# Kernel optimization log

Hardware: AMD Instinct MI355X
Metric: run time of the kernel (lower is better)

The kernel has to match this reference:

```python
import jax, jax.numpy as jnp
import numpy as np

T, B, D, H, F, E = 2048, 2, 1024, 16, 4096, 8
HD = D // H


def layer_norm(x, g, b, eps=1e-5):
    m = x.mean(-1, keepdims=True)
    v = ((x - m) ** 2).mean(-1, keepdims=True)
    return (x - m) * jax.lax.rsqrt(v + eps) * g + b


def setup_inputs() -> dict:
    key = jax.random.key(0)
    ks = jax.random.split(key, 24)
    s = 0.02
    inp = {
        "x": jax.random.normal(ks[0], (T, B, D), jnp.float32),
        # self-attention (fairseq MultiheadAttention)
        "Wq": jax.random.normal(ks[1], (D, D), jnp.float32) * s,
        "bq": jnp.zeros((D,), jnp.float32),
        "Wk": jax.random.normal(ks[2], (D, D), jnp.float32) * s,
        "bk": jnp.zeros((D,), jnp.float32),
        "Wv": jax.random.normal(ks[3], (D, D), jnp.float32) * s,
        "bv": jnp.zeros((D,), jnp.float32),
        "Wo": jax.random.normal(ks[4], (D, D), jnp.float32) * s,
        "bo": jnp.zeros((D,), jnp.float32),
        "ln1_g": jnp.ones((D,), jnp.float32),
        "ln1_b": jnp.zeros((D,), jnp.float32),
        "ln2_g": jnp.ones((D,), jnp.float32),
        "ln2_b": jnp.zeros((D,), jnp.float32),
        # MoE: expert_centroids Linear(D -> E, bias=False) => weight [E, D]
        "cent": jax.random.normal(ks[5], (E, D), jnp.float32) * s,
        # per-expert MoESublayer params (base_sublayers=1)
        "e_ln_g": jnp.ones((E, D), jnp.float32),
        "e_ln_b": jnp.zeros((E, D), jnp.float32),
        "e_W1": jax.random.normal(ks[6], (E, D, F), jnp.float32) * s,
        "e_b1": jnp.zeros((E, F), jnp.float32),
        "e_W2": jax.random.normal(ks[7], (E, F, D), jnp.float32) * s,
        "e_b2": jnp.zeros((E, D), jnp.float32),
    }
    return inp


def reference(x, Wq, bq, Wk, bk, Wv, bv, Wo, bo, ln1_g, ln1_b, ln2_g, ln2_b,
              cent, e_ln_g, e_ln_b, e_W1, e_b1, e_W2, e_b2):
    # ---- self-attention block (pre-norm, causal) ----
    res = x  # [T,B,D]
    h = layer_norm(x, ln1_g, ln1_b)
    q = ((h @ Wq) + bq) * (HD ** -0.5)
    k = h @ Wk + bk
    v = h @ Wv + bv
    q = q.reshape(T, B, H, HD)
    k = k.reshape(T, B, H, HD)
    v = v.reshape(T, B, H, HD)
    scores = jnp.einsum('tbhd,sbhd->bhts', q, k)
    causal = jnp.tril(jnp.ones((T, T), bool))
    scores = jnp.where(causal, scores, -1e9)
    p = jax.nn.softmax(scores, axis=-1)
    a = jnp.einsum('bhts,sbhd->tbhd', p, v).reshape(T, B, D)
    x = res + (a @ Wo + bo)

    # ---- MoE block (pre-norm) ----
    res = x
    h = layer_norm(x, ln2_g, ln2_b)
    # MoELayer: transpose(0,1) then flatten -> [B*T, D] token-major by batch
    xs = h.transpose(1, 0, 2).reshape(B * T, D)
    logits = xs.astype(jnp.float32) @ cent.T  # fp32 gating, [N,E]
    assign = jnp.argmax(logits, axis=-1)      # greedy top-1 routing

    # single-device semantics: All2All identity; sort + inverse-sort cancel,
    # so out[t] = expert_{assign[t]}(xs[t]). Compute each expert densely and select.
    def sublayer(g, b, W1, b1, W2, b2):
        hh = jax.nn.relu(layer_norm(xs, g, b) @ W1 + b1)  # [N,F]
        return xs + hh @ W2 + b2                          # internal residual

    ys = jax.vmap(sublayer)(e_ln_g, e_ln_b, e_W1, e_b1, e_W2, e_b2)  # [E,N,D]
    moe_out = jnp.take_along_axis(ys, assign[None, :, None], axis=0)[0]  # [N,D]
    moe_out = moe_out.reshape(B, T, D).transpose(1, 0, 2)  # back to [T,B,D]

    return res + moe_out
```

## Files before the change

kernel.cpp:

```cpp
#include <hip/hip_runtime.h>
#include <hip/hip_bf16.h>
#include <math.h>

#define T_ 2048
#define B_ 2
#define D_ 1024
#define H_ 16
#define F_ 4096
#define E_ 8
#define N_ 4096
#define HD_ 64
#define PADROWS 5120

typedef __attribute__((ext_vector_type(8))) short short8_t;
typedef __attribute__((ext_vector_type(4))) float f32x4_t;
typedef __attribute__((ext_vector_type(16))) float f32x16_t;
typedef __attribute__((ext_vector_type(4))) unsigned u32x4_t;

__device__ __forceinline__ unsigned short f2bf(float f) {
    union { float f; unsigned u; } a; a.f = f;
    unsigned r = a.u + 0x7FFFu + ((a.u >> 16) & 1u);
    return (unsigned short)(r >> 16);
}

__device__ __forceinline__ unsigned cvtpk(float lo, float hi) {
    unsigned r;
    asm("v_cvt_pk_bf16_f32 %0, %1, %2" : "=v"(r) : "v"(lo), "v"(hi));
    return r;
}

__device__ __forceinline__ void glds16(const unsigned short* g, unsigned short* l) {
    __builtin_amdgcn_global_load_lds(
        (const __attribute__((address_space(1))) void*)g,
        (__attribute__((address_space(3))) void*)l, 16, 0, 0);
}

__device__ __forceinline__ void blockReduce2(float& a, float& b, float* sm) {
    #pragma unroll
    for (int m = 32; m; m >>= 1) { a += __shfl_xor(a, m); b += __shfl_xor(b, m); }
    const int w = threadIdx.x >> 6, l = threadIdx.x & 63;
    __syncthreads();
    if (l == 0) { sm[w] = a; sm[8 + w] = b; }
    __syncthreads();
    a = sm[0] + sm[1] + sm[2] + sm[3];
    b = sm[8] + sm[9] + sm[10] + sm[11];
}

__global__ __launch_bounds__(256) void k_transpose(const float* __restrict__ in,
                                                   unsigned short* __restrict__ out,
                                                   int R, int C) {
    __shared__ float tile[32][33];
    const int c0 = blockIdx.x * 32, r0 = blockIdx.y * 32;
    const size_t base = (size_t)blockIdx.z * R * C;
    in += base; out += base;
    const int tx = threadIdx.x & 31, ty = threadIdx.x >> 5;
    #pragma unroll
    for (int i = 0; i < 32; i += 8)
        tile[ty + i][tx] = in[(size_t)(r0 + ty + i) * C + c0 + tx];
    __syncthreads();
    const int c = threadIdx.x >> 3, rq = (threadIdx.x & 7) * 4;
    ushort4 v;
    v.x = f2bf(tile[rq + 0][c]);
    v.y = f2bf(tile[rq + 1][c]);
    v.z = f2bf(tile[rq + 2][c]);
    v.w = f2bf(tile[rq + 3][c]);
    *(ushort4*)(out + (size_t)(c0 + c) * R + r0 + rq) = v;
}

__global__ __launch_bounds__(256) void k_transpose_v(const unsigned short* __restrict__ in,
                                                     unsigned short* __restrict__ out) {
    const int bh = blockIdx.x;
    const int t0 = blockIdx.y * 128;
    const int tid = threadIdx.x;
    const int hd = tid & 63;
    const size_t ib = (size_t)bh * T_ * HD_;
    const size_t ob = (size_t)bh * HD_ * T_;
    for (int tb = tid >> 6; tb < 16; tb += 4) {
        const int t = t0 + tb * 8;
        short8_t v;
        #pragma unroll
        for (int k = 0; k < 8; ++k)
            v[k] = (short)in[ib + (size_t)(t + k) * HD_ + hd];
        *(short8_t*)(out + ob + (size_t)hd * T_ + t) = v;
    }
}

__global__ __launch_bounds__(256) void k_ln(const float* __restrict__ x,
                                            const float* __restrict__ g,
                                            const float* __restrict__ b,
                                            unsigned short* __restrict__ out) {
    __shared__ float sm[16];
    const int row = blockIdx.x, tid = threadIdx.x;
    const float4 v = *(const float4*)(x + (size_t)row * D_ + tid * 4);
    float s1 = v.x + v.y + v.z + v.w;
    float s2 = v.x * v.x + v.y * v.y + v.z * v.z + v.w * v.w;
    blockReduce2(s1, s2, sm);
    const float mean = s1 * (1.f / D_);
    const float inv  = rsqrtf(s2 * (1.f / D_) - mean * mean + 1e-5f);
    const float4 gg = *(const float4*)(g + tid * 4);
    const float4 bb = *(const float4*)(b + tid * 4);
    unsigned long long pk =
          (unsigned long long)f2bf((v.x - mean) * inv * gg.x + bb.x)
        | ((unsigned long long)f2bf((v.y - mean) * inv * gg.y + bb.y) << 16)
        | ((unsigned long long)f2bf((v.z - mean) * inv * gg.z + bb.z) << 32)
        | ((unsigned long long)f2bf((v.w - mean) * inv * gg.w + bb.w) << 48);
    *(unsigned long long*)(out + (size_t)row * D_ + tid * 4) = pk;
}

__global__ __launch_bounds__(256) void k_init_x2(const float* __restrict__ x,
                                                 const float* __restrict__ bo,
                                                 float* __restrict__ x2) {
    const int row = blockIdx.x, tid = threadIdx.x;
    const size_t idx = (size_t)row * D_ + tid * 4;
    const float4 v = *(const float4*)(x + idx);
    const float4 b = *(const float4*)(bo + tid * 4);
    float4 o; o.x = v.x + b.x; o.y = v.y + b.y; o.z = v.z + b.z; o.w = v.w + b.w;
    *(float4*)(x2 + idx) = o;
}

__global__ __launch_bounds__(256) void k_init_out(const float* __restrict__ x2u,
                                                  const float* __restrict__ eb2,
                                                  const int* __restrict__ assign,
                                                  float* __restrict__ out) {
    const int row = blockIdx.x, tid = threadIdx.x;
    const int e = assign[row];
    const size_t idx = (size_t)row * D_ + tid * 4;
    const float4 v = *(const float4*)(x2u + idx);
    const float4 b = *(const float4*)(eb2 + (size_t)e * D_ + tid * 4);
    float4 o; o.x = v.x + b.x; o.y = v.y + b.y; o.z = v.z + b.z; o.w = v.w + b.w;
    *(float4*)(out + idx) = o;
}

__device__ __forceinline__ void gemm_core(const unsigned short* ap0, const unsigned short* ap1,
                                          const unsigned short* bp0, const unsigned short* bp1,
                                          int K, unsigned short* Als, unsigned short* Bls,
                                          f32x4_t (&acc)[4][4]) {
    const int tid = threadIdx.x, w = tid >> 6, l = tid & 63;
    const int wm = (w >> 1) * 64, wn = (w & 1) * 64;
    const int fr = l & 15, fg = (l >> 4) * 8;
    const int fgs = fg ^ (((fr >> 1) & 3) << 3);
    f32x4_t z4 = {0.f, 0.f, 0.f, 0.f};
    #pragma unroll
    for (int m = 0; m < 4; m++)
        #pragma unroll
        for (int n = 0; n < 4; n++) acc[m][n] = z4;
    glds16(ap0, Als + w * 512);
    glds16(ap1, Als + (w + 4) * 512);
    glds16(bp0, Bls + w * 512);
    glds16(bp1, Bls + (w + 4) * 512);
    ap0 += 32; ap1 += 32; bp0 += 32; bp1 += 32;
    glds16(ap0, Als + 4096 + w * 512);
    glds16(ap1, Als + 4096 + (w + 4) * 512);
    glds16(bp0, Bls + 4096 + w * 512);
    glds16(bp1, Bls + 4096 + (w + 4) * 512);
    ap0 += 32; ap1 += 32; bp0 += 32; bp1 += 32;
    unsigned c0 = 0, c1 = 4096, c2 = 8192;
    const int nk = K >> 5;
    for (int kt = 0; kt < nk; ++kt) {
        if (kt < nk - 1) asm volatile("s_waitcnt vmcnt(4)" ::: "memory");
        else             asm volatile("s_waitcnt vmcnt(0)" ::: "memory");
        __builtin_amdgcn_s_barrier();
        __builtin_amdgcn_sched_barrier(0);
        short8_t a[4], b[4];
        #pragma unroll
        for (int m = 0; m < 4; m++) a[m] = *(const short8_t*)(Als + c0 + (wm + m * 16 + fr) * 32 + fgs);
        #pragma unroll
        for (int n = 0; n < 4; n++) b[n] = *(const short8_t*)(Bls + c0 + (wn + n * 16 + fr) * 32 + fgs);
        #pragma unroll
        for (int m = 0; m < 4; m++)
            #pragma unroll
            for (int n = 0; n < 4; n++)
                acc[m][n] = __builtin_amdgcn_mfma_f32_16x16x32_bf16(a[m], b[n], acc[m][n], 0, 0, 0);
        if (kt + 2 < nk) {
            glds16(ap0, Als + c2 + w * 512);
            glds16(ap1, Als + c2 + (w + 4) * 512);
            glds16(bp0, Bls + c2 + w * 512);
            glds16(bp1, Bls + c2 + (w + 4) * 512);
            ap0 += 32; ap1 += 32; bp0 += 32; bp1 += 32;
        }
        const unsigned t = c0; c0 = c1; c1 = c2; c2 = t;
    }
}

__global__ __launch_bounds__(256) void k_gemm_qkv(
    const unsigned short* __restrict__ A, const unsigned short* __restrict__ BT,
    const float* __restrict__ bq, const float* __restrict__ bk, const float* __restrict__ bv,
    unsigned short* __restrict__ Qb, unsigned short* __restrict__ Kb, unsigned short* __restrict__ Vb) {
    __shared__ unsigned short Als[12288], Bls[12288];
    const int tid = threadIdx.x, w = tid >> 6, l = tid & 63;
    const int col0 = blockIdx.x * 128, row0 = blockIdx.y * 128;
    const int r0s = w * 16 + (l >> 2), r1s = 64 + w * 16 + (l >> 2);
    const int cs = ((l & 3) ^ ((l >> 3) & 3)) * 8;
    const unsigned short* ap0 = A + (size_t)(row0 + r0s) * D_ + cs;
    const unsigned short* ap1 = A + (size_t)(row0 + r1s) * D_ + cs;
    const unsigned short* bp0 = BT + (size_t)(col0 + r0s) * D_ + cs;
    const unsigned short* bp1 = BT + (size_t)(col0 + r1s) * D_ + cs;
    f32x4_t acc[4][4];
    gemm_core(ap0, ap1, bp0, bp1, D_, Als, Bls, acc);
    const int wm = (w >> 1) * 64, wn = (w & 1) * 64, fr = l & 15, fg4 = l >> 4;
    #pragma unroll
    for (int n = 0; n < 4; n++) {
        const int gcol = col0 + wn + n * 16 + fr;
        const int which = gcol >> 10, dc = gcol & 1023;
        const float bias = which == 0 ? bq[dc] : (which == 1 ? bk[dc] : bv[dc]);
        unsigned short* dst = which == 0 ? Qb : (which == 1 ? Kb : Vb);
        const int hh = dc >> 6, hd = dc & 63;
        #pragma unroll
        for (int m = 0; m < 4; m++)
            #pragma unroll
            for (int rr = 0; rr < 4; rr++) {
                const int grow = row0 + wm + m * 16 + fg4 * 4 + rr;
                float v = acc[m][n][rr] + bias;
                if (which == 0) v *= 0.1803368801111204f;
                const int t = grow >> 1, bb = grow & 1;
                dst[((size_t)(bb * H_ + hh) * T_ + t) * HD_ + hd] = f2bf(v);
            }
    }
}

__global__ __launch_bounds__(256) void k_attn(const unsigned short* __restrict__ Qb,
                                              const unsigned short* __restrict__ Kb,
                                              const unsigned short* __restrict__ Vt,
                                              unsigned short* __restrict__ aout) {
    __shared__ unsigned short Kl[3 * 4096];
    __shared__ unsigned short Vl[3 * 4096];
    const int id = blockIdx.x;
    const int qt = (id < 256) ? (15 - (id & 15)) : (id & 15);
    const int bh = (id >> 4) & 31;
    const int tid = threadIdx.x, w = tid >> 6, l = tid & 63;
    const int q5 = l & 31, hi = l >> 5, l7 = l & 7;
    const int row0 = w * 8 + (l >> 3);
    const int swz = ((l & 7) ^ (l >> 3)) * 8;
    const size_t base = (size_t)bh * T_ * HD_;
    const unsigned short* Qp = Qb + base;
    const unsigned short* kps = Kb + base + (size_t)row0 * HD_ + swz;
    const unsigned short* vps = Vt + base + (size_t)row0 * T_ + swz;
    const int qw0 = qt * 128 + w * 32;
    const int q = qw0 + q5;

    short8_t aq[4];
    #pragma unroll
    for (int khd = 0; khd < 4; ++khd)
        aq[khd] = *(const short8_t*)(Qp + (size_t)q * HD_ + khd * 16 + hi * 8);

    f32x16_t accO0, accO1;
    #pragma unroll
    for (int i = 0; i < 16; ++i) { accO0[i] = 0.f; accO1[i] = 0.f; }
    float mrun = -1e30f, lrun = 0.f;

    const int niter = (qt + 1) * 2;

#define STAGE_KV(t, b) { \
    const size_t ko = (size_t)(t) * 64 * HD_; const int vo = (t) * 64; \
    glds16(kps + ko,            Kl + (b) + w * 512); \
    glds16(kps + ko + 32 * HD_, Kl + (b) + 2048 + w * 512); \
    glds16(vps + vo,            Vl + (b) + w * 512); \
    glds16(vps + vo + 32 * T_,  Vl + (b) + 2048 + w * 512); }

    STAGE_KV(0, 0);
    STAGE_KV(1, 4096);
    unsigned c0 = 0, c1 = 4096, c2 = 8192;

    for (int it = 0; it < niter; ++it) {
        if (it < niter - 1) asm volatile("s_waitcnt vmcnt(4)" ::: "memory");
        else                asm volatile("s_waitcnt vmcnt(0)" ::: "memory");
        __builtin_amdgcn_s_barrier();
        __builtin_amdgcn_sched_barrier(0);
        const int s0 = it * 64;
        if (s0 <= qw0 + 31) {
            const unsigned short* KT = Kl + c0;
            const unsigned short* VT = Vl + c0;

            f32x16_t st0, st1;
            #pragma unroll
            for (int i = 0; i < 16; ++i) { st0[i] = 0.f; st1[i] = 0.f; }
            #pragma unroll
            for (int khd = 0; khd < 4; ++khd) {
                const int cb = (khd * 16 + hi * 8) ^ (l7 * 8);
                const short8_t k0 = *(const short8_t*)(KT + q5 * 64 + cb);
                const short8_t k1 = *(const short8_t*)(KT + (32 + q5) * 64 + cb);
                st0 = __builtin_amdgcn_mfma_f32_32x32x16_bf16(k0, aq[khd], st0, 0, 0, 0);
                st1 = __builtin_amdgcn_mfma_f32_32x32x16_bf16(k1, aq[khd], st1, 0, 0, 0);
            }

            const bool domask = (s0 + 63 > qw0);
            float pmax = -3e38f;
            #pragma unroll
            for (int r = 0; r < 16; ++r) {
                float v0 = st0[r], v1 = st1[r];
                if (domask) {
                    const int kv0 = s0 + (r & 3) + 8 * (r >> 2) + 4 * hi;
                    if (kv0 > q)      v0 = -1e30f;
                    if (kv0 + 32 > q) v1 = -1e30f;
                }
                st0[r] = v0; st1[r] = v1;
                pmax = fmaxf(pmax, fmaxf(v0, v1));
            }
            pmax = fmaxf(pmax, __shfl_xor(pmax, 32));
            const float mnew = fmaxf(mrun, pmax);
            const float scl = exp2f(mrun - mnew);
            float pt0[16], pt1[16];
            float rs = 0.f;
            #pragma unroll
            for (int r = 0; r < 16; ++r) {
                pt0[r] = exp2f(st0[r] - mnew);
                pt1[r] = exp2f(st1[r] - mnew);
                rs += pt0[r] + pt1[r];
            }
            rs += __shfl_xor(rs, 32);
            lrun = lrun * scl + rs;
            mrun = mnew;
            #pragma unroll
            for (int i = 0; i < 16; ++i) { accO0[i] *= scl; accO1[i] *= scl; }

            unsigned Wp[2][4][2];
            #pragma unroll
            for (int b = 0; b < 4; ++b) {
                Wp[0][b][0] = cvtpk(pt0[4 * b + 0], pt0[4 * b + 1]);
                Wp[0][b][1] = cvtpk(pt0[4 * b + 2], pt0[4 * b + 3]);
                Wp[1][b][0] = cvtpk(pt1[4 * b + 0], pt1[4 * b + 1]);
                Wp[1][b][1] = cvtpk(pt1[4 * b + 2], pt1[4 * b + 3]);
            }

            #pragma unroll
            for (int ks = 0; ks < 4; ++ks) {
                const int t = ks >> 1, b0 = (ks & 1) * 2;
                const unsigned ownA0 = Wp[t][b0][0],     ownA1 = Wp[t][b0][1];
                const unsigned ownB0 = Wp[t][b0 + 1][0], ownB1 = Wp[t][b0 + 1][1];
                const unsigned send0 = hi ? ownA0 : ownB0;
                const unsigned send1 = hi ? ownA1 : ownB1;
                const unsigned recv0 = __shfl_xor(send0, 32);
                const unsigned recv1 = __shfl_xor(send1, 32);
                u32x4_t wds;
                wds[0] = hi ? recv0 : ownA0;
                wds[1] = hi ? recv1 : ownA1;
                wds[2] = hi ? ownB0 : recv0;
                wds[3] = hi ? ownB1 : recv1;
                const short8_t pfrag = __builtin_bit_cast(short8_t, wds);
                const int cb = (ks * 16 + hi * 8) ^ (l7 * 8);
                const short8_t v0 = *(const short8_t*)(VT + q5 * 64 + cb);
                const short8_t v1 = *(const short8_t*)(VT + (32 + q5) * 64 + cb);
                accO0 = __builtin_amdgcn_mfma_f32_32x32x16_bf16(v0, pfrag, accO0, 0, 0, 0);
                accO1 = __builtin_amdgcn_mfma_f32_32x32x16_bf16(v1, pfrag, accO1, 0, 0, 0);
            }
        }
        if (it + 2 < niter) STAGE_KV(it + 2, c2);
        const unsigned tb = c0; c0 = c1; c1 = c2; c2 = tb;
    }
#undef STAGE_KV

    const float linv = 1.f / lrun;
    const int bidx = bh >> 4, hidx = bh & 15;
    unsigned short* orow = aout + (size_t)(q * B_ + bidx) * D_ + hidx * 64;
    #pragma unroll
    for (int g = 0; g < 4; ++g) {
        const int hd0 = 8 * g + 4 * hi;
        unsigned long long pk0 =
              (unsigned long long)f2bf(accO0[4 * g + 0] * linv)
            | ((unsigned long long)f2bf(accO0[4 * g + 1] * linv) << 16)
            | ((unsigned long long)f2bf(accO0[4 * g + 2] * linv) << 32)
            | ((unsigned long long)f2bf(accO0[4 * g + 3] * linv) << 48);
        *(unsigned long long*)(orow + hd0) = pk0;
        unsigned long long pk1 =
              (unsigned long long)f2bf(accO1[4 * g + 0] * linv)
            | ((unsigned long long)f2bf(accO1[4 * g + 1] * linv) << 16)
            | ((unsigned long long)f2bf(accO1[4 * g + 2] * linv) << 32)
            | ((unsigned long long)f2bf(accO1[4 * g + 3] * linv) << 48);
        *(unsigned long long*)(orow + 32 + hd0) = pk1;
    }
}

__global__ __launch_bounds__(256) void k_gemm_o(
    const unsigned short* __restrict__ A, const unsigned short* __restrict__ BT,
    float* __restrict__ x2) {
    __shared__ unsigned short Als[12288], Bls[12288];
    const int tid = threadIdx.x, w = tid >> 6, l = tid & 63;
    const int row0 = blockIdx.x * 128, col0 = blockIdx.y * 128;
    const int kc = blockIdx.z * 512;
    const int r0s = w * 16 + (l >> 2), r1s = 64 + w * 16 + (l >> 2);
    const int cs = ((l & 3) ^ ((l >> 3) & 3)) * 8;
    const unsigned short* ap0 = A + (size_t)(row0 + r0s) * D_ + kc + cs;
    const unsigned short* ap1 = A + (size_t)(row0 + r1s) * D_ + kc + cs;
    const unsigned short* bp0 = BT + (size_t)(col0 + r0s) * D_ + kc + cs;
    const unsigned short* bp1 = BT + (size_t)(col0 + r1s) * D_ + kc + cs;
    f32x4_t acc[4][4];
    gemm_core(ap0, ap1, bp0, bp1, 512, Als, Bls, acc);
    const int wm = (w >> 1) * 64, wn = (w & 1) * 64, fr = l & 15, fg4 = l >> 4;
    #pragma unroll
    for (int n = 0; n < 4; n++) {
        const int gcol = col0 + wn + n * 16 + fr;
        #pragma unroll
        for (int m = 0; m < 4; m++)
            #pragma unroll
            for (int rr = 0; rr < 4; rr++) {
                const int grow = row0 + wm + m * 16 + fg4 * 4 + rr;
                atomicAdd(&x2[(size_t)grow * D_ + gcol], acc[m][n][rr]);
            }
    }
}

__global__ __launch_bounds__(256) void k_ln2_gate(
    float* __restrict__ x2, const float* __restrict__ g2, const float* __restrict__ b2,
    const float* __restrict__ cent, const float* __restrict__ eg, const float* __restrict__ eb,
    unsigned short* __restrict__ z, int* __restrict__ assign, int* __restrict__ counts) {
    __shared__ float sm[48];
    const int row = blockIdx.x, tid = threadIdx.x;
    const int w = tid >> 6, l = tid & 63;
    float* xr = x2 + (size_t)row * D_;
    const float4 v = *(const float4*)(xr + tid * 4);
    float s1 = v.x + v.y + v.z + v.w;
    float s2 = v.x * v.x + v.y * v.y + v.z * v.z + v.w * v.w;
    blockReduce2(s1, s2, sm);
    const float mean = s1 * (1.f / D_);
    const float inv  = rsqrtf(s2 * (1.f / D_) - mean * mean + 1e-5f);
    const float4 gg = *(const float4*)(g2 + tid * 4), bb = *(const float4*)(b2 + tid * 4);
    float4 u;
    u.x = (v.x - mean) * inv * gg.x + bb.x;
    u.y = (v.y - mean) * inv * gg.y + bb.y;
    u.z = (v.z - mean) * inv * gg.z + bb.z;
    u.w = (v.w - mean) * inv * gg.w + bb.w;
    float p[E_];
    #pragma unroll
    for (int e = 0; e < E_; e++) {
        const float4 c = *(const float4*)(cent + (size_t)e * D_ + tid * 4);
        p[e] = u.x * c.x + u.y * c.y + u.z * c.z + u.w * c.w;
    }
    #pragma unroll
    for (int m = 32; m; m >>= 1)
        #pragma unroll
        for (int e = 0; e < E_; e++) p[e] += __shfl_xor(p[e], m);
    __syncthreads();
    if (l == 0) {
        #pragma unroll
        for (int e = 0; e < E_; e++) sm[16 + e * 4 + w] = p[e];
    }
    __syncthreads();
    int best = 0; float bl = -1e30f;
    #pragma unroll
    for (int e = 0; e < E_; e++) {
        const float le = sm[16 + e * 4] + sm[16 + e * 4 + 1] + sm[16 + e * 4 + 2] + sm[16 + e * 4 + 3];
        if (le > bl) { bl = le; best = e; }
    }
    float t1 = u.x + u.y + u.z + u.w;
    float t2 = u.x * u.x + u.y * u.y + u.z * u.z + u.w * u.w;
    blockReduce2(t1, t2, sm);
    const float m2   = t1 * (1.f / D_);
    const float inv2 = rsqrtf(t2 * (1.f / D_) - m2 * m2 + 1e-5f);
    const float4 egv = *(const float4*)(eg + (size_t)best * D_ + tid * 4);
    const float4 ebv = *(const float4*)(eb + (size_t)best * D_ + tid * 4);
    unsigned long long pk =
          (unsigned long long)f2bf((u.x - m2) * inv2 * egv.x + ebv.x)
        | ((unsigned long long)f2bf((u.y - m2) * inv2 * egv.y + ebv.y) << 16)
        | ((unsigned long long)f2bf((u.z - m2) * inv2 * egv.z + ebv.z) << 32)
        | ((unsigned long long)f2bf((u.w - m2) * inv2 * egv.w + ebv.w) << 48);
    *(unsigned long long*)(z + (size_t)row * D_ + tid * 4) = pk;
    float4 xu; xu.x = v.x + u.x; xu.y = v.y + u.y; xu.z = v.z + u.z; xu.w = v.w + u.w;
    *(float4*)(xr + tid * 4) = xu;
    if (tid == 0) { assign[row] = best; atomicAdd(&counts[best], 1); }
}

__global__ void k_init(int* counts, int* cursor, int* perm) {
    const int t = threadIdx.x;
    if (t < E_) { counts[t] = 0; cursor[t] = 0; }
    for (int i = t; i < PADROWS; i += 256) perm[i] = -1;
}

__global__ void k_offsets(const int* counts, int* pad_off) {
    if (threadIdx.x == 0) {
        int o = 0; pad_off[0] = 0;
        for (int e = 0; e < E_; e++) { o += ((counts[e] + 127) >> 7) << 7; pad_off[e + 1] = o; }
    }
}

__global__ void k_scatter(const int* assign, const int* pad_off, int* cursor, int* perm) {
    const int r = blockIdx.x * 256 + threadIdx.x;
    if (r >= N_) return;
    const int e = assign[r];
    const int pos = pad_off[e] + atomicAdd(&cursor[e], 1);
    perm[pos] = r;
}

__global__ __launch_bounds__(256) void k_gemm_e1(
    const unsigned short* __restrict__ z, const unsigned short* __restrict__ W1T,
    const float* __restrict__ eb1, const int* __restrict__ pad_off,
    const int* __restrict__ perm, unsigned short* __restrict__ Y1) {
    __shared__ unsigned short Als[12288], Bls[12288];
    const int tid = threadIdx.x, w = tid >> 6, l = tid & 63;
    const int col0 = blockIdx.x * 128, row0 = blockIdx.y * 128;
    if (row0 >= pad_off[E_]) return;
    int e = 0;
    while (row0 >= pad_off[e + 1]) e++;
    const int r0s = w * 16 + (l >> 2), r1s = 64 + w * 16 + (l >> 2);
    const int cs = ((l & 3) ^ ((l >> 3) & 3)) * 8;
    int pr0 = perm[row0 + r0s]; if (pr0 < 0) pr0 = 0;
    int pr1 = perm[row0 + r1s]; if (pr1 < 0) pr1 = 0;
    const unsigned short* ap0 = z + (size_t)pr0 * D_ + cs;
    const unsigned short* ap1 = z + (size_t)pr1 * D_ + cs;
    const unsigned short* BTe = W1T + (size_t)e * F_ * D_;
    const unsigned short* bp0 = BTe + (size_t)(col0 + r0s) * D_ + cs;
    const unsigned short* bp1 = BTe + (size_t)(col0 + r1s) * D_ + cs;
    f32x4_t acc[4][4];
    gemm_core(ap0, ap1, bp0, bp1, D_, Als, Bls, acc);
    const float* b1e = eb1 + (size_t)e * F_;
    const int wm = (w >> 1) * 64, wn = (w & 1) * 64, fr = l & 15, fg4 = l >> 4;
    #pragma unroll
    for (int n = 0; n < 4; n++) {
        const int gcol = col0 + wn + n * 16 + fr;
        const float bias = b1e[gcol];
        #pragma unroll
        for (int m = 0; m < 4; m++)
            #pragma unroll
            for (int rr = 0; rr < 4; rr++) {
                const int grow = row0 + wm + m * 16 + fg4 * 4 + rr;
                Y1[(size_t)grow * F_ + gcol] = f2bf(fmaxf(acc[m][n][rr] + bias, 0.f));
            }
    }
}

__global__ __launch_bounds__(256) void k_gemm_e2(
    const unsigned short* __restrict__ Y1, const unsigned short* __restrict__ W2T,
    const int* __restrict__ pad_off, const int* __restrict__ perm,
    float* __restrict__ out) {
    __shared__ unsigned short Als[12288], Bls[12288];
    const int tid = threadIdx.x, w = tid >> 6, l = tid & 63;
    const int row0 = blockIdx.x * 128, col0 = blockIdx.y * 128;
    const int kc = blockIdx.z * 2048;
    if (row0 >= pad_off[E_]) return;
    int e = 0;
    while (row0 >= pad_off[e + 1]) e++;
    const int r0s = w * 16 + (l >> 2), r1s = 64 + w * 16 + (l >> 2);
    const int cs = ((l & 3) ^ ((l >> 3) & 3)) * 8;
    const unsigned short* ap0 = Y1 + (size_t)(row0 + r0s) * F_ + kc + cs;
    const unsigned short* ap1 = Y1 + (size_t)(row0 + r1s) * F_ + kc + cs;
    const unsigned short* BTe = W2T + (size_t)e * D_ * F_;
    const unsigned short* bp0 = BTe + (size_t)(col0 + r0s) * F_ + kc + cs;
    const unsigned short* bp1 = BTe + (size_t)(col0 + r1s) * F_ + kc + cs;
    f32x4_t acc[4][4];
    gemm_core(ap0, ap1, bp0, bp1, 2048, Als, Bls, acc);
    const int wm = (w >> 1) * 64, wn = (w & 1) * 64, fr = l & 15, fg4 = l >> 4;
    #pragma unroll
    for (int n = 0; n < 4; n++) {
        const int gcol = col0 + wn + n * 16 + fr;
        #pragma unroll
        for (int m = 0; m < 4; m++)
            #pragma unroll
            for (int rr = 0; rr < 4; rr++) {
                const int grow = row0 + wm + m * 16 + fg4 * 4 + rr;
                const int rdst = perm[grow];
                if (rdst >= 0)
                    atomicAdd(&out[(size_t)rdst * D_ + gcol], acc[m][n][rr]);
            }
    }
}

extern "C" void kernel_launch(void* const* d_in, const int* in_sizes, int n_in,
                              void* d_out, int out_size, void* d_ws, size_t ws_size,
                              hipStream_t stream) {
    const float* x    = (const float*)d_in[0];
    const float* Wq   = (const float*)d_in[1];
    const float* bq   = (const float*)d_in[2];
    const float* Wk   = (const float*)d_in[3];
    const float* bk   = (const float*)d_in[4];
    const float* Wv   = (const float*)d_in[5];
    const float* bv   = (const float*)d_in[6];
    const float* Wo   = (const float*)d_in[7];
    const float* bo   = (const float*)d_in[8];
    const float* ln1g = (const float*)d_in[9];
    const float* ln1b = (const float*)d_in[10];
    const float* ln2g = (const float*)d_in[11];
    const float* ln2b = (const float*)d_in[12];
    const float* cent = (const float*)d_in[13];
    const float* egw  = (const float*)d_in[14];
    const float* ebw  = (const float*)d_in[15];
    const float* eW1  = (const float*)d_in[16];
    const float* eb1  = (const float*)d_in[17];
    const float* eW2  = (const float*)d_in[18];
    const float* eb2  = (const float*)d_in[19];
    float* out = (float*)d_out;

    char* W = (char*)d_ws;
    unsigned short* WqkvT = (unsigned short*)(W);
    unsigned short* WoT   = (unsigned short*)(W + 6291456);
    unsigned short* Qb    = (unsigned short*)(W + 8388608);
    unsigned short* Kb    = (unsigned short*)(W + 16777216);
    unsigned short* Vb    = (unsigned short*)(W + 25165824);
    unsigned short* aout  = (unsigned short*)(W + 33554432);
    unsigned short* Y1    = (unsigned short*)(W);
    unsigned short* W1T   = (unsigned short*)(W + 41943040);
    unsigned short* W2T   = (unsigned short*)(W + 109051904);
    unsigned short* h1z   = (unsigned short*)(W + 176160768);
    float*          x2    = (float*)(W + 184549376);
    unsigned short* Vt    = (unsigned short*)(W + 201326592);
    int*            assign= (int*)(W + 209715200);
    int*            perm  = (int*)(W + 209731584);
    int*            counts= (int*)(W + 209752064);
    int*            cursor= (int*)(W + 209752192);
    int*            pad_off=(int*)(W + 209752320);

    k_transpose<<<dim3(32, 32, 1), 256, 0, stream>>>(Wq, WqkvT,               1024, 1024);
    k_transpose<<<dim3(32, 32, 1), 256, 0, stream>>>(Wk, WqkvT + 1024 * 1024, 1024, 1024);
    k_transpose<<<dim3(32, 32, 1), 256, 0, stream>>>(Wv, WqkvT + 2048 * 1024, 1024, 1024);
    k_transpose<<<dim3(32, 32, 1), 256, 0, stream>>>(Wo, WoT,                 1024, 1024);
    k_transpose<<<dim3(128, 32, 8), 256, 0, stream>>>(eW1, W1T, 1024, 4096);
    k_transpose<<<dim3(32, 128, 8), 256, 0, stream>>>(eW2, W2T, 4096, 1024);

    k_init<<<1, 256, 0, stream>>>(counts, cursor, perm);
    k_ln<<<N_, 256, 0, stream>>>(x, ln1g, ln1b, h1z);
    k_init_x2<<<N_, 256, 0, stream>>>(x, bo, x2);
    k_gemm_qkv<<<dim3(24, 32), 256, 0, stream>>>(h1z, WqkvT, bq, bk, bv, Qb, Kb, Vb);
    k_transpose_v<<<dim3(32, 16), 256, 0, stream>>>(Vb, Vt);
    k_attn<<<dim3(512), 256, 0, stream>>>(Qb, Kb, Vt, aout);
    k_gemm_o<<<dim3(32, 8, 2), 256, 0, stream>>>(aout, WoT, x2);
    k_ln2_gate<<<N_, 256, 0, stream>>>(x2, ln2g, ln2b, cent, egw, ebw, h1z, assign, counts);
    k_offsets<<<1, 64, 0, stream>>>(counts, pad_off);
    k_scatter<<<16, 256, 0, stream>>>(assign, pad_off, cursor, perm);
    k_init_out<<<N_, 256, 0, stream>>>(x2, eb2, assign, out);
    k_gemm_e1<<<dim3(32, 40), 256, 0, stream>>>(h1z, W1T, eb1, pad_off, perm, Y1);
    k_gemm_e2<<<dim3(40, 8, 2), 256, 0, stream>>>(Y1, W2T, pad_off, perm, out);
}
```

Measured before the change: 486.8 us.

## Fuse small launches, issue prefetch before MFMA, and raise MFMA wave priority

Merges the four attention-weight transposes into one launch, and folds the init and x2-bias kernels into the first layernorm kernel. In the GEMM core and the attention loop, the next-stage global-to-LDS prefetch is now issued before the MFMA block instead of after it. The MFMA sections are wrapped in s_setprio so matrix waves get scheduling priority. This targets launch overhead and poor overlap of memory traffic with compute. The risk is that issuing the prefetch earlier overwrites a buffer slot other waves may still be reading, although the triple-buffer rotation appears to keep it safe.

Result: no change. 481.3 us (-1.1%).

```diff
diff --git a/kernel.cpp b/kernel.cpp
--- a/kernel.cpp
+++ b/kernel.cpp
@@ -44,6 +44,29 @@
     __syncthreads();
     a = sm[0] + sm[1] + sm[2] + sm[3];
     b = sm[8] + sm[9] + sm[10] + sm[11];
+}
+
+__global__ __launch_bounds__(256) void k_transpose4(
+    const float* __restrict__ Wq, const float* __restrict__ Wk,
+    const float* __restrict__ Wv, const float* __restrict__ Wo,
+    unsigned short* __restrict__ WqkvT, unsigned short* __restrict__ WoT) {
+    __shared__ float tile[32][33];
+    const int zi = blockIdx.z;
+    const float* in = zi == 0 ? Wq : (zi == 1 ? Wk : (zi == 2 ? Wv : Wo));
+    unsigned short* out = zi == 3 ? WoT : (WqkvT + (size_t)zi * 1024 * 1024);
+    const int c0 = blockIdx.x * 32, r0 = blockIdx.y * 32;
+    const int tx = threadIdx.x & 31, ty = threadIdx.x >> 5;
+    #pragma unroll
+    for (int i = 0; i < 32; i += 8)
+        tile[ty + i][tx] = in[(size_t)(r0 + ty + i) * 1024 + c0 + tx];
+    __syncthreads();
+    const int c = threadIdx.x >> 3, rq = (threadIdx.x & 7) * 4;
+    ushort4 v;
+    v.x = f2bf(tile[rq + 0][c]);
+    v.y = f2bf(tile[rq + 1][c]);
+    v.z = f2bf(tile[rq + 2][c]);
+    v.w = f2bf(tile[rq + 3][c]);
+    *(ushort4*)(out + (size_t)(c0 + c) * 1024 + r0 + rq) = v;
 }
 
 __global__ __launch_bounds__(256) void k_transpose(const float* __restrict__ in,
@@ -85,12 +108,20 @@
     }
 }
 
-__global__ __launch_bounds__(256) void k_ln(const float* __restrict__ x,
-                                            const float* __restrict__ g,
-                                            const float* __restrict__ b,
-                                            unsigned short* __restrict__ out) {
+__global__ __launch_bounds__(256) void k_ln_x2(const float* __restrict__ x,
+                                               const float* __restrict__ g,
+                                               const float* __restrict__ b,
+                                               const float* __restrict__ bo,
+                                               unsigned short* __restrict__ out,
+                                               float* __restrict__ x2,
+                                               int* __restrict__ counts, int* __restrict__ cursor,
+                                               int* __restrict__ perm) {
     __shared__ float sm[16];
     const int row = blockIdx.x, tid = threadIdx.x;
+    if (row == 0) {
+        if (tid < E_) { counts[tid] = 0; cursor[tid] = 0; }
+        for (int i = tid; i < PADROWS; i += 256) perm[i] = -1;
+    }
     const float4 v = *(const float4*)(x + (size_t)row * D_ + tid * 4);
     float s1 = v.x + v.y + v.z + v.w;
     float s2 = v.x * v.x + v.y * v.y + v.z * v.z + v.w * v.w;
@@ -105,17 +136,9 @@
         | ((unsigned long long)f2bf((v.z - mean) * inv * gg.z + bb.z) << 32)
         | ((unsigned long long)f2bf((v.w - mean) * inv * gg.w + bb.w) << 48);
     *(unsigned long long*)(out + (size_t)row * D_ + tid * 4) = pk;
-}
-
-__global__ __launch_bounds__(256) void k_init_x2(const float* __restrict__ x,
-                                                 const float* __restrict__ bo,
-                                                 float* __restrict__ x2) {
-    const int row = blockIdx.x, tid = threadIdx.x;
-    const size_t idx = (size_t)row * D_ + tid * 4;
-    const float4 v = *(const float4*)(x + idx);
-    const float4 b = *(const float4*)(bo + tid * 4);
-    float4 o; o.x = v.x + b.x; o.y = v.y + b.y; o.z = v.z + b.z; o.w = v.w + b.w;
-    *(float4*)(x2 + idx) = o;
+    const float4 bv = *(const float4*)(bo + tid * 4);
+    float4 o; o.x = v.x + bv.x; o.y = v.y + bv.y; o.z = v.z + bv.z; o.w = v.w + bv.w;
+    *(float4*)(x2 + (size_t)row * D_ + tid * 4) = o;
 }
 
 __global__ __launch_bounds__(256) void k_init_out(const float* __restrict__ x2u,
@@ -161,16 +184,6 @@
         else             asm volatile("s_waitcnt vmcnt(0)" ::: "memory");
         __builtin_amdgcn_s_barrier();
         __builtin_amdgcn_sched_barrier(0);
-        short8_t a[4], b[4];
-        #pragma unroll
-        for (int m = 0; m < 4; m++) a[m] = *(const short8_t*)(Als + c0 + (wm + m * 16 + fr) * 32 + fgs);
-        #pragma unroll
-        for (int n = 0; n < 4; n++) b[n] = *(const short8_t*)(Bls + c0 + (wn + n * 16 + fr) * 32 + fgs);
-        #pragma unroll
-        for (int m = 0; m < 4; m++)
-            #pragma unroll
-            for (int n = 0; n < 4; n++)
-                acc[m][n] = __builtin_amdgcn_mfma_f32_16x16x32_bf16(a[m], b[n], acc[m][n], 0, 0, 0);
         if (kt + 2 < nk) {
             glds16(ap0, Als + c2 + w * 512);
             glds16(ap1, Als + c2 + (w + 4) * 512);
@@ -178,6 +191,18 @@
             glds16(bp1, Bls + c2 + (w + 4) * 512);
             ap0 += 32; ap1 += 32; bp0 += 32; bp1 += 32;
         }
+        short8_t a[4], b[4];
+        #pragma unroll
+        for (int m = 0; m < 4; m++) a[m] = *(const short8_t*)(Als + c0 + (wm + m * 16 + fr) * 32 + fgs);
+        #pragma unroll
+        for (int n = 0; n < 4; n++) b[n] = *(const short8_t*)(Bls + c0 + (wn + n * 16 + fr) * 32 + fgs);
+        __builtin_amdgcn_s_setprio(1);
+        #pragma unroll
+        for (int m = 0; m < 4; m++)
+            #pragma unroll
+            for (int n = 0; n < 4; n++)
+                acc[m][n] = __builtin_amdgcn_mfma_f32_16x16x32_bf16(a[m], b[n], acc[m][n], 0, 0, 0);
+        __builtin_amdgcn_s_setprio(0);
         const unsigned t = c0; c0 = c1; c1 = c2; c2 = t;
     }
 }
@@ -266,6 +291,7 @@
         else                asm volatile("s_waitcnt vmcnt(0)" ::: "memory");
         __builtin_amdgcn_s_barrier();
         __builtin_amdgcn_sched_barrier(0);
+        if (it + 2 < niter) STAGE_KV(it + 2, c2);
         const int s0 = it * 64;
         if (s0 <= qw0 + 31) {
             const unsigned short* KT = Kl + c0;
@@ -274,6 +300,7 @@
             f32x16_t st0, st1;
             #pragma unroll
             for (int i = 0; i < 16; ++i) { st0[i] = 0.f; st1[i] = 0.f; }
+            __builtin_amdgcn_s_setprio(1);
             #pragma unroll
             for (int khd = 0; khd < 4; ++khd) {
                 const int cb = (khd * 16 + hi * 8) ^ (l7 * 8);
@@ -282,6 +309,7 @@
                 st0 = __builtin_amdgcn_mfma_f32_32x32x16_bf16(k0, aq[khd], st0, 0, 0, 0);
                 st1 = __builtin_amdgcn_mfma_f32_32x32x16_bf16(k1, aq[khd], st1, 0, 0, 0);
             }
+            __builtin_amdgcn_s_setprio(0);
 
             const bool domask = (s0 + 63 > qw0);
             float pmax = -3e38f;
@@ -322,6 +350,7 @@
                 Wp[1][b][1] = cvtpk(pt1[4 * b + 2], pt1[4 * b + 3]);
             }
 
+            __builtin_amdgcn_s_setprio(1);
             #pragma unroll
             for (int ks = 0; ks < 4; ++ks) {
                 const int t = ks >> 1, b0 = (ks & 1) * 2;
@@ -343,8 +372,8 @@
                 accO0 = __builtin_amdgcn_mfma_f32_32x32x16_bf16(v0, pfrag, accO0, 0, 0, 0);
                 accO1 = __builtin_amdgcn_mfma_f32_32x32x16_bf16(v1, pfrag, accO1, 0, 0, 0);
             }
+            __builtin_amdgcn_s_setprio(0);
         }
-        if (it + 2 < niter) STAGE_KV(it + 2, c2);
         const unsigned tb = c0; c0 = c1; c1 = c2; c2 = tb;
     }
 #undef STAGE_KV
@@ -457,12 +486,6 @@
     float4 xu; xu.x = v.x + u.x; xu.y = v.y + u.y; xu.z = v.z + u.z; xu.w = v.w + u.w;
     *(float4*)(xr + tid * 4) = xu;
     if (tid == 0) { assign[row] = best; atomicAdd(&counts[best], 1); }
-}
-
-__global__ void k_init(int* counts, int* cursor, int* perm) {
-    const int t = threadIdx.x;
-    if (t < E_) { counts[t] = 0; cursor[t] = 0; }
-    for (int i = t; i < PADROWS; i += 256) perm[i] = -1;
 }
 
 __global__ void k_offsets(const int* counts, int* pad_off) {
@@ -597,16 +620,11 @@
     int*            cursor= (int*)(W + 209752192);
     int*            pad_off=(int*)(W + 209752320);
 
-    k_transpose<<<dim3(32, 32, 1), 256, 0, stream>>>(Wq, WqkvT,               1024, 1024);
-    k_transpose<<<dim3(32, 32, 1), 256, 0, stream>>>(Wk, WqkvT + 1024 * 1024, 1024, 1024);
-    k_transpose<<<dim3(32, 32, 1), 256, 0, stream>>>(Wv, WqkvT + 2048 * 1024, 1024, 1024);
-    k_transpose<<<dim3(32, 32, 1), 256, 0, stream>>>(Wo, WoT,                 1024, 1024);
+    k_transpose4<<<dim3(32, 32, 4), 256, 0, stream>>>(Wq, Wk, Wv, Wo, WqkvT, WoT);
     k_transpose<<<dim3(128, 32, 8), 256, 0, stream>>>(eW1, W1T, 1024, 4096);
     k_transpose<<<dim3(32, 128, 8), 256, 0, stream>>>(eW2, W2T, 4096, 1024);
 
-    k_init<<<1, 256, 0, stream>>>(counts, cursor, perm);
-    k_ln<<<N_, 256, 0, stream>>>(x, ln1g, ln1b, h1z);
-    k_init_x2<<<N_, 256, 0, stream>>>(x, bo, x2);
+    k_ln_x2<<<N_, 256, 0, stream>>>(x, ln1g, ln1b, bo, h1z, x2, counts, cursor, perm);
     k_gemm_qkv<<<dim3(24, 32), 256, 0, stream>>>(h1z, WqkvT, bq, bk, bv, Qb, Kb, Vb);
     k_transpose_v<<<dim3(32, 16), 256, 0, stream>>>(Vb, Vt);
     k_attn<<<dim3(512), 256, 0, stream>>>(Qb, Kb, Vt, aout);
```
